# Optimization experiments

Hardware: AMD Instinct MI355X
Metric: run time of the kernel (lower is better)

The kernel has to match this reference:

```python
import jax, jax.numpy as jnp
import numpy as np

VOCAB_SIZE = 13
EMBED_DIM = 50
HIDDEN_DIM = 50
BATCH = 2048
SEQ_LEN = 2048


def setup_inputs() -> dict:
    key = jax.random.key(0)
    ks = jax.random.split(key, 10)
    s = 0.1
    return {
        "x": jax.random.randint(ks[0], (BATCH, SEQ_LEN), 0, VOCAB_SIZE),
        "embed": jax.random.normal(ks[1], (VOCAB_SIZE, EMBED_DIM), jnp.float32),
        "W_ih": jax.random.normal(ks[2], (4 * HIDDEN_DIM, EMBED_DIM), jnp.float32) * s,
        "W_hh": jax.random.normal(ks[3], (4 * HIDDEN_DIM, HIDDEN_DIM), jnp.float32) * s,
        "b_ih": jax.random.normal(ks[4], (4 * HIDDEN_DIM,), jnp.float32) * s,
        "b_hh": jax.random.normal(ks[5], (4 * HIDDEN_DIM,), jnp.float32) * s,
        "W1": jax.random.normal(ks[6], (HIDDEN_DIM, HIDDEN_DIM), jnp.float32) * s,
        "b1": jax.random.normal(ks[7], (HIDDEN_DIM,), jnp.float32) * s,
        "W2": jax.random.normal(ks[8], (1, HIDDEN_DIM), jnp.float32) * s,
        "b2": jax.random.normal(ks[9], (1,), jnp.float32) * s,
    }


def reference(x, embed, W_ih, W_hh, b_ih, b_hh, W1, b1, W2, b2):
    B = x.shape[0]
    H = HIDDEN_DIM
    embeds = embed[x]                    # [B, T, E]
    xs = jnp.swapaxes(embeds, 0, 1)      # [T, B, E] for scan over time

    def step(carry, xt):
        hx, cx = carry
        gates = xt @ W_ih.T + b_ih + hx @ W_hh.T + b_hh   # [B, 4H]
        i = jax.nn.sigmoid(gates[:, 0 * H:1 * H])
        f = jax.nn.sigmoid(gates[:, 1 * H:2 * H])
        g = jnp.tanh(gates[:, 2 * H:3 * H])
        o = jax.nn.sigmoid(gates[:, 3 * H:4 * H])
        cx = f * cx + i * g
        hx = o * jnp.tanh(cx)
        return (hx, cx), None

    init = (jnp.zeros((B, H), embeds.dtype), jnp.zeros((B, H), embeds.dtype))
    (hx, _), _ = jax.lax.scan(step, init, xs)

    h = jax.nn.relu(hx @ W1.T + b1)
    out = (h @ W2.T + b2).squeeze(1)     # [B]
    return out
```

## Files before the change

### kernel.cpp

```cpp
#include <hip/hip_runtime.h>
#include <hip/hip_fp16.h>

#define T_SEQ 2048
#define HID   50
#define KP    64
#define MB    8
#define NBLK  256
#define NTHR  512
#define HSTR  80
#define BUFB  (MB*HSTR)

#define NLOG2E  1.4426950408889634f
#define N2LOG2E 2.8853900817779268f

typedef __attribute__((ext_vector_type(8))) _Float16 half8;
typedef __attribute__((ext_vector_type(4))) float    f32x4;

__device__ __forceinline__ ushort f16b(float f){ return __half_as_ushort(__float2half(f)); }
__device__ __forceinline__ float rcp_(float x){ return __builtin_amdgcn_rcpf(x); }
__device__ __forceinline__ float ex2_(float x){ return __builtin_amdgcn_exp2f(x); }
__device__ __forceinline__ float dpp_swap8(float v){
    return __int_as_float(__builtin_amdgcn_mov_dpp(__float_as_int(v), 0x128, 0xF, 0xF, true));
}

__global__ void build_B(const float* __restrict__ embed, const float* __restrict__ Wih,
                        const float* __restrict__ Whh, const float* __restrict__ bih,
                        const float* __restrict__ bhh, ushort* __restrict__ Bm) {
    int idx = blockIdx.x * blockDim.x + threadIdx.x;
    if (idx >= 256 * KP) return;
    int col = idx >> 6, k = idx & 63;
    int w = col >> 5, j = (col >> 4) & 1, cc = col & 15;
    int g = 2 * j + (cc >> 3);
    int u = 8 * w + (cc & 7);
    ushort v = 0;
    if (u < HID) {
        int r = g * HID + u;
        float s = (g == 2) ? -N2LOG2E : -NLOG2E;
        if (k < HID) {
            v = f16b(s * Whh[r * HID + k]);
        } else if (k < 63) {
            float t = 0.f;
            for (int e = 0; e < HID; ++e)
                t = fmaf(embed[(k - 50) * HID + e], Wih[r * HID + e], t);
            v = f16b(s * t);
        } else {
            v = f16b(s * (bih[r] + bhh[r]));
        }
    }
    Bm[idx] = v;
}

__global__ __launch_bounds__(NTHR, 2) void lstm8w(
    const int*    __restrict__ x,
    const ushort* __restrict__ Bm,
    const float*  __restrict__ W1,
    const float*  __restrict__ b1,
    const float*  __restrict__ W2,
    const float*  __restrict__ b2,
    float*        __restrict__ out)
{
    const int t    = threadIdx.x;
    const int w    = t >> 6;
    const int l    = t & 63;
    const int q    = l >> 4;
    const int c16  = l & 15;
    const bool lo  = (c16 < 8);
    const int u    = 8 * w + (c16 & 7);
    const int myrow = 2 * q + (lo ? 0 : 1);
    const int wu   = __builtin_amdgcn_readfirstlane(w);

    __shared__ __align__(16) ushort hbuf[2 * BUFB];
    __shared__ float zb[HID * MB];

    half8 bf[2][2];
    {
        const ushort* bp = Bm + (w * 32 + c16) * KP + q * 8;
        #pragma unroll
        for (int j = 0; j < 2; ++j) {
            bf[j][0] = *(const half8*)(bp + j * 16 * KP);
            bf[j][1] = *(const half8*)(bp + j * 16 * KP + 32);
        }
    }
    asm volatile("" : "+v"(bf[0][0]), "+v"(bf[0][1]), "+v"(bf[1][0]), "+v"(bf[1][1]));

    for (int i = t; i < 2 * BUFB; i += NTHR) hbuf[i] = 0;

    const int* xw = x + ((long)blockIdx.x * MB + wu) * T_SEQ;
    int tk0 = xw[0];
    int tk1 = xw[1];
    __syncthreads();
    if (l == 0) {
        hbuf[0 * BUFB + wu * HSTR + 63] = 0x3C00;
        hbuf[1 * BUFB + wu * HSTR + 63] = 0x3C00;
        hbuf[0 * BUFB + wu * HSTR + 50 + tk0] = 0x3C00;
        hbuf[1 * BUFB + wu * HSTR + 50 + tk1] = 0x3C00;
    }
    int t0r = tk1, t1r = tk0, t2r = tk1;
    __syncthreads();

    const ushort* ar  = hbuf + (c16 >> 1) * HSTR + q * 8;
    ushort*       wr_ = hbuf + myrow * HSTR + u;
    ushort*       hbw = hbuf + wu * HSTR + 50;

    float cs = 0.f;

#define MFMA_(A,B,C) __builtin_amdgcn_mfma_f32_16x16x32_f16((A),(B),(C),0,0,0)
#define STEP(P) do {                                                              \
        int it = step + 2 + (P); if (it > T_SEQ - 1) it = T_SEQ - 1;              \
        int tn = xw[it];                             \
        half8 a0 = *(const half8*)(ar + (P) * BUFB);                              \
        half8 a1 = *(const half8*)(ar + (P) * BUFB + 32);                         \
        const f32x4 zz = {0.f, 0.f, 0.f, 0.f};                                    \
        __builtin_amdgcn_s_setprio(1);                                            \
        f32x4 z0 = MFMA_(a0, bf[0][0], zz);                                       \
        z0 = MFMA_(a1, bf[0][1], z0);              \
        f32x4 z1 = MFMA_(a0, bf[1][0], zz);                                       \
        z1 = MFMA_(a1, bf[1][1], z1);                                             \
        __builtin_amdgcn_s_setprio(0);                                            \
        float s0l = z0[0];                               \
        float s0h = z0[2];                               \
        float s1l = z1[0];                               \
        float s1h = z1[2];                               \
        float rx0 = dpp_swap8(lo ? s0h : s0l);    \
        float rx1 = dpp_swap8(lo ? s1h : s1l);                                    \
        float gi = lo ? s0l : rx0;                  \
        float gf = lo ? rx0 : s0h;                                                \
        float gg = lo ? s1l : rx1;                                                \
        float go = lo ? rx1 : s1h;                                                \
               \
        float pi = ex2_(gi);                                                      \
        float pf = ex2_(gf);                                                      \
        float qg = ex2_(gg);                                                      \
        float Df = 1.f + pf;                                                      \
        float D2 = (1.f + pi) * (1.f + qg);                                       \
        float ivA = rcp_(Df * D2);                                                \
        float fv  = ivA * D2;                                       \
        float igs = ivA * Df * fmaf(N2LOG2E, qg, -N2LOG2E);      \
        cs = fmaf(fv, cs, igs);                                                   \
        float po = ex2_(go);                                                      \
        float qc = ex2_(fminf(cs, 30.f));       \
        float ivB = rcp_((1.f + po) * (1.f + qc));                                \
        float hh  = ivB * (1.f - qc);                       \
        if (u < HID) wr_[(1 - (P)) * BUFB] = f16b(hh);                            \
        if (l == 0) {                                                             \
            ushort* hb = hbw + (1 - (P)) * BUFB;                                  \
            hb[t0r] = 0;                                                          \
            hb[t2r] = 0x3C00;                                                     \
        }                                                                         \
        t0r = t1r; t1r = t2r; t2r = tn;                          \
        __syncthreads();                                                          \
    } while (0)

    #pragma unroll 1
    for (int step = 0; step < T_SEQ; step += 2) {
        STEP(0);
        STEP(1);
    }
#undef STEP
#undef MFMA_

    if (t < MB * HID) {
        int m = t & 7, uu = t >> 3;
        float a = b1[uu];
        const ushort* hr = hbuf + m * HSTR;
        #pragma unroll 10
        for (int k = 0; k < HID; ++k)
            a = fmaf(W1[uu * HID + k], __half2float(__ushort_as_half(hr[k])), a);
        zb[uu * MB + m] = fmaxf(a, 0.f);
    }
    __syncthreads();
    if (t < MB) {
        float a = b2[0];
        #pragma unroll 10
        for (int j = 0; j < HID; ++j)
            a = fmaf(W2[j], zb[j * MB + t], a);
        out[blockIdx.x * MB + t] = a;
    }
}

extern "C" void kernel_launch(void* const* d_in, const int* in_sizes, int n_in,
                              void* d_out, int out_size, void* d_ws, size_t ws_size,
                              hipStream_t stream) {
    const int*   x     = (const int*)  d_in[0];
    const float* embed = (const float*)d_in[1];
    const float* W_ih  = (const float*)d_in[2];
    const float* W_hh  = (const float*)d_in[3];
    const float* b_ih  = (const float*)d_in[4];
    const float* b_hh  = (const float*)d_in[5];
    const float* W1    = (const float*)d_in[6];
    const float* b1    = (const float*)d_in[7];
    const float* W2    = (const float*)d_in[8];
    const float* b2    = (const float*)d_in[9];
    float* out = (float*)d_out;

    ushort* Bm = (ushort*)d_ws;

    build_B<<<(256 * KP + 255) / 256, 256, 0, stream>>>(
        embed, W_ih, W_hh, b_ih, b_hh, Bm);

    lstm8w<<<NBLK, NTHR, 0, stream>>>(
        x, Bm, W1, b1, W2, b2, out);
}
```

Measured before the change: 703.9 us.

## Use four waves per block with each wave covering sixteen hidden units and all gates

```diff
diff --git a/kernel.cpp b/kernel.cpp
--- a/kernel.cpp
+++ b/kernel.cpp
@@ -6,7 +6,7 @@
 #define KP    64
 #define MB    8
 #define NBLK  256
-#define NTHR  512
+#define NTHR  256
 #define HSTR  80
 #define BUFB  (MB*HSTR)
 
@@ -19,9 +19,6 @@
 __device__ __forceinline__ ushort f16b(float f){ return __half_as_ushort(__float2half(f)); }
 __device__ __forceinline__ float rcp_(float x){ return __builtin_amdgcn_rcpf(x); }
 __device__ __forceinline__ float ex2_(float x){ return __builtin_amdgcn_exp2f(x); }
-__device__ __forceinline__ float dpp_swap8(float v){
-    return __int_as_float(__builtin_amdgcn_mov_dpp(__float_as_int(v), 0x128, 0xF, 0xF, true));
-}
 
 __global__ void build_B(const float* __restrict__ embed, const float* __restrict__ Wih,
                         const float* __restrict__ Whh, const float* __restrict__ bih,
@@ -29,9 +26,8 @@
     int idx = blockIdx.x * blockDim.x + threadIdx.x;
     if (idx >= 256 * KP) return;
     int col = idx >> 6, k = idx & 63;
-    int w = col >> 5, j = (col >> 4) & 1, cc = col & 15;
-    int g = 2 * j + (cc >> 3);
-    int u = 8 * w + (cc & 7);
+    int wq = col >> 6, g = (col >> 4) & 3, cc = col & 15;
+    int u = wq * 16 + cc;
     ushort v = 0;
     if (u < HID) {
         int r = g * HID + u;
@@ -50,7 +46,7 @@
     Bm[idx] = v;
 }
 
-__global__ __launch_bounds__(NTHR, 2) void lstm8w(
+__global__ __launch_bounds__(NTHR, 1) void lstm4w(
     const int*    __restrict__ x,
     const ushort* __restrict__ Bm,
     const float*  __restrict__ W1,
@@ -64,90 +60,100 @@
     const int l    = t & 63;
     const int q    = l >> 4;
     const int c16  = l & 15;
-    const bool lo  = (c16 < 8);
-    const int u    = 8 * w + (c16 & 7);
-    const int myrow = 2 * q + (lo ? 0 : 1);
+    const int u    = 16 * w + c16;
+    const int upos = (u < HID) ? u : (64 + u - HID);
     const int wu   = __builtin_amdgcn_readfirstlane(w);
 
     __shared__ __align__(16) ushort hbuf[2 * BUFB];
     __shared__ float zb[HID * MB];
 
-    half8 bf[2][2];
+    half8 bf[4][2];
     {
-        const ushort* bp = Bm + (w * 32 + c16) * KP + q * 8;
+        const ushort* bp = Bm + (w * 64 + c16) * KP + q * 8;
         #pragma unroll
-        for (int j = 0; j < 2; ++j) {
-            bf[j][0] = *(const half8*)(bp + j * 16 * KP);
-            bf[j][1] = *(const half8*)(bp + j * 16 * KP + 32);
+        for (int g = 0; g < 4; ++g) {
+            bf[g][0] = *(const half8*)(bp + g * 16 * KP);
+            bf[g][1] = *(const half8*)(bp + g * 16 * KP + 32);
         }
     }
-    asm volatile("" : "+v"(bf[0][0]), "+v"(bf[0][1]), "+v"(bf[1][0]), "+v"(bf[1][1]));
+    #pragma unroll
+    for (int g = 0; g < 4; ++g)
+        asm volatile("" : "+v"(bf[g][0]), "+v"(bf[g][1]));
 
     for (int i = t; i < 2 * BUFB; i += NTHR) hbuf[i] = 0;
 
-    const int* xw = x + ((long)blockIdx.x * MB + wu) * T_SEQ;
-    int tk0 = xw[0];
-    int tk1 = xw[1];
+    const int row0 = blockIdx.x * MB;
     __syncthreads();
-    if (l == 0) {
-        hbuf[0 * BUFB + wu * HSTR + 63] = 0x3C00;
-        hbuf[1 * BUFB + wu * HSTR + 63] = 0x3C00;
-        hbuf[0 * BUFB + wu * HSTR + 50 + tk0] = 0x3C00;
-        hbuf[1 * BUFB + wu * HSTR + 50 + tk1] = 0x3C00;
-    }
-    int t0r = tk1, t1r = tk0, t2r = tk1;
+    if (t < MB) {
+        int tk0 = x[(long)(row0 + t) * T_SEQ + 0];
+        int tk1 = x[(long)(row0 + t) * T_SEQ + 1];
+        hbuf[0 * BUFB + t * HSTR + 63] = 0x3C00;
+        hbuf[1 * BUFB + t * HSTR + 63] = 0x3C00;
+        hbuf[0 * BUFB + t * HSTR + 50 + tk0] = 0x3C00;
+        hbuf[1 * BUFB + t * HSTR + 50 + tk1] = 0x3C00;
+    }
     __syncthreads();
 
+    const int* xA = x + (long)(row0 + wu) * T_SEQ;
+    const int* xB = x + (long)(row0 + 4 + wu) * T_SEQ;
+    int tA0 = xA[1], tA1 = xA[0], tA2 = xA[1];
+    int tB0 = xB[1], tB1 = xB[0], tB2 = xB[1];
+
     const ushort* ar  = hbuf + (c16 >> 1) * HSTR + q * 8;
-    ushort*       wr_ = hbuf + myrow * HSTR + u;
-    ushort*       hbw = hbuf + wu * HSTR + 50;
-
-    float cs = 0.f;
+    ushort*       wr_ = hbuf + (2 * q) * HSTR + upos;
+
+    float cs0 = 0.f, cs1 = 0.f;
 
 #define MFMA_(A,B,C) __builtin_amdgcn_mfma_f32_16x16x32_f16((A),(B),(C),0,0,0)
-#define STEP(P) do {                                                              \
-        int it = step + 2 + (P); if (it > T_SEQ - 1) it = T_SEQ - 1;              \
-        int tn = xw[it];                             \
-        half8 a0 = *(const half8*)(ar + (P) * BUFB);                              \
-        half8 a1 = *(const half8*)(ar + (P) * BUFB + 32);                         \
-        const f32x4 zz = {0.f, 0.f, 0.f, 0.f};                                    \
-        __builtin_amdgcn_s_setprio(1);                                            \
-        f32x4 z0 = MFMA_(a0, bf[0][0], zz);                                       \
-        z0 = MFMA_(a1, bf[0][1], z0);              \
-        f32x4 z1 = MFMA_(a0, bf[1][0], zz);                                       \
-        z1 = MFMA_(a1, bf[1][1], z1);                                             \
-        __builtin_amdgcn_s_setprio(0);                                            \
-        float s0l = z0[0];                               \
-        float s0h = z0[2];                               \
-        float s1l = z1[0];                               \
-        float s1h = z1[2];                               \
-        float rx0 = dpp_swap8(lo ? s0h : s0l);    \
-        float rx1 = dpp_swap8(lo ? s1h : s1l);                                    \
-        float gi = lo ? s0l : rx0;                  \
-        float gf = lo ? rx0 : s0h;                                                \
-        float gg = lo ? s1l : rx1;                                                \
-        float go = lo ? rx1 : s1h;                                                \
-               \
-        float pi = ex2_(gi);                                                      \
-        float pf = ex2_(gf);                                                      \
-        float qg = ex2_(gg);                                                      \
+#define ACT(GI,GF,GG,GO,CS,HH) do {                                               \
+        float pi = ex2_(GI);                                                      \
+        float pf = ex2_(GF);                                                      \
+        float qg = ex2_(GG);                                                      \
         float Df = 1.f + pf;                                                      \
         float D2 = (1.f + pi) * (1.f + qg);                                       \
         float ivA = rcp_(Df * D2);                                                \
-        float fv  = ivA * D2;                                       \
-        float igs = ivA * Df * fmaf(N2LOG2E, qg, -N2LOG2E);      \
-        cs = fmaf(fv, cs, igs);                                                   \
-        float po = ex2_(go);                                                      \
-        float qc = ex2_(fminf(cs, 30.f));       \
+        float fv  = ivA * D2;                                                     \
+        float igs = ivA * Df * fmaf(N2LOG2E, qg, -N2LOG2E);                       \
+        CS = fmaf(fv, CS, igs);                                                   \
+        float po = ex2_(GO);                                                      \
+        float qc = ex2_(fminf(CS, 30.f));                                         \
         float ivB = rcp_((1.f + po) * (1.f + qc));                                \
-        float hh  = ivB * (1.f - qc);                       \
-        if (u < HID) wr_[(1 - (P)) * BUFB] = f16b(hh);                            \
-        if (l == 0) {                                                             \
-            ushort* hb = hbw + (1 - (P)) * BUFB;                                  \
-            hb[t0r] = 0;                                                          \
-            hb[t2r] = 0x3C00;                                                     \
+        HH = ivB * (1.f - qc);                                                    \
+    } while (0)
+
+#define STEP(P) do {                                                              \
+        half8 a0 = *(const half8*)(ar + (P) * BUFB);        \
+        half8 a1 = *(const half8*)(ar + (P) * BUFB + 32);                         \
+        int it = step + 2 + (P); if (it > T_SEQ - 1) it = T_SEQ - 1;              \
+        int tnA = xA[it];                                    \
+        int tnB = xB[it];                                                         \
+        const f32x4 zz = {0.f, 0.f, 0.f, 0.f};                                    \
+        f32x4 zA0 = MFMA_(a0, bf[0][0], zz);             \
+        f32x4 zB0 = MFMA_(a1, bf[0][1], zz);                                      \
+        f32x4 zA1 = MFMA_(a0, bf[1][0], zz);                                      \
+        f32x4 zB1 = MFMA_(a1, bf[1][1], zz);                                      \
+        f32x4 zA2 = MFMA_(a0, bf[2][0], zz);                                      \
+        f32x4 zB2 = MFMA_(a1, bf[2][1], zz);                                      \
+        f32x4 zA3 = MFMA_(a0, bf[3][0], zz);                                      \
+        f32x4 zB3 = MFMA_(a1, bf[3][1], zz);                                      \
+        float gi0 = zA0[0] + zB0[0], gi1 = zA0[2] + zB0[2];                       \
+        float gf0 = zA1[0] + zB1[0], gf1 = zA1[2] + zB1[2];                       \
+        float gg0 = zA2[0] + zB2[0], gg1 = zA2[2] + zB2[2];                       \
+        float go0 = zA3[0] + zB3[0], go1 = zA3[2] + zB3[2];                       \
+        float h0, h1;                                                             \
+        ACT(gi0, gf0, gg0, go0, cs0, h0);                           \
+        ACT(gi1, gf1, gg1, go1, cs1, h1);                           \
+        wr_[(1 - (P)) * BUFB]        = f16b(h0);                                  \
+        wr_[(1 - (P)) * BUFB + HSTR] = f16b(h1);                                  \
+        if (l == 0) {                          \
+            ushort* hb = hbuf + (1 - (P)) * BUFB;                                 \
+            hb[wu * HSTR + 50 + tA0] = 0;                                         \
+            hb[wu * HSTR + 50 + tA2] = 0x3C00;                                    \
+            hb[(4 + wu) * HSTR + 50 + tB0] = 0;                                   \
+            hb[(4 + wu) * HSTR + 50 + tB2] = 0x3C00;                              \
         }                                                                         \
-        t0r = t1r; t1r = t2r; t2r = tn;                          \
+        tA0 = tA1; tA1 = tA2; tA2 = tnA;                                          \
+        tB0 = tB1; tB1 = tB2; tB2 = tnB;                                          \
         __syncthreads();                                                          \
     } while (0)
 
@@ -157,10 +163,11 @@
         STEP(1);
     }
 #undef STEP
+#undef ACT
 #undef MFMA_
 
-    if (t < MB * HID) {
-        int m = t & 7, uu = t >> 3;
+    for (int idx = t; idx < MB * HID; idx += NTHR) {
+        int m = idx & 7, uu = idx >> 3;
         float a = b1[uu];
         const ushort* hr = hbuf + m * HSTR;
         #pragma unroll 10
@@ -174,7 +181,7 @@
         #pragma unroll 10
         for (int j = 0; j < HID; ++j)
             a = fmaf(W2[j], zb[j * MB + t], a);
-        out[blockIdx.x * MB + t] = a;
+        out[row0 + t] = a;
     }
 }
 
@@ -198,6 +205,6 @@
     build_B<<<(256 * KP + 255) / 256, 256, 0, stream>>>(
         embed, W_ih, W_hh, b_ih, b_hh, Bm);
 
-    lstm8w<<<NBLK, NTHR, 0, stream>>>(
+    lstm4w<<<NBLK, NTHR, 0, stream>>>(
         x, Bm, W1, b1, W2, b2, out);
 }
```

Result: slower. 776.3 us (+10.3%).
